# Kernel optimization log

Measured on AMD Instinct MI355X. Metric: run time of the kernel, lower is better.

Reference implementation:

```python
import jax, jax.numpy as jnp
import numpy as np

N_NODES = 50000
N_EDGES = 500000
D = 128  # in_size == out_size


def setup_inputs() -> dict:
    key = jax.random.key(0)
    ks = jax.random.split(key, 12)
    s = 1.0 / np.sqrt(D)
    feats = jax.random.normal(ks[0], (N_NODES, D), dtype=jnp.float32)
    # per-etype Linear params (torch Linear: y = x @ W.T + b)
    W_chem = jax.random.uniform(ks[1], (D, D), jnp.float32, -s, s)
    b_chem = jax.random.uniform(ks[2], (D,), jnp.float32, -s, s)
    W_elec = jax.random.uniform(ks[3], (D, D), jnp.float32, -s, s)
    b_elec = jax.random.uniform(ks[4], (D,), jnp.float32, -s, s)
    W_out = jax.random.uniform(ks[5], (D, D), jnp.float32, -s, s)
    b_out = jax.random.uniform(ks[6], (D,), jnp.float32, -s, s)
    src_chem = jax.random.randint(ks[7], (N_EDGES,), 0, N_NODES, dtype=jnp.int32)
    dst_chem = jax.random.randint(ks[8], (N_EDGES,), 0, N_NODES, dtype=jnp.int32)
    src_elec = jax.random.randint(ks[9], (N_EDGES,), 0, N_NODES, dtype=jnp.int32)
    dst_elec = jax.random.randint(ks[10], (N_EDGES,), 0, N_NODES, dtype=jnp.int32)
    return {
        "feats": feats,
        "W_chem": W_chem, "b_chem": b_chem,
        "W_elec": W_elec, "b_elec": b_elec,
        "W_out": W_out, "b_out": b_out,
        "src_chem": src_chem, "dst_chem": dst_chem,
        "src_elec": src_elec, "dst_elec": dst_elec,
    }


def reference(feats, W_chem, b_chem, W_elec, b_elec, W_out, b_out,
              src_chem, dst_chem, src_elec, dst_elec):
    n = feats.shape[0]
    # Per-etype linear projection of all node features
    Wh_chem = feats @ W_chem.T + b_chem  # [N, D]
    Wh_elec = feats @ W_elec.T + b_elec  # [N, D]
    # copy_src + sum scatter-aggregation per etype, merged with 'sum'
    h = jax.ops.segment_sum(Wh_chem[src_chem], dst_chem, num_segments=n)
    h = h + jax.ops.segment_sum(Wh_elec[src_elec], dst_elec, num_segments=n)
    # output Linear plus the last-iterated etype's Wh (quirk of original code:
    # 'electrical' is last in etypes order)
    return h @ W_out.T + b_out + Wh_elec
```

## Files before the change

### kernel.cpp

```cpp
#include <hip/hip_runtime.h>

#define D 128
#define PAD 48

typedef __attribute__((ext_vector_type(8))) short bf16x8;
typedef __attribute__((ext_vector_type(4))) float f32x4;

__device__ __forceinline__ unsigned short f2bf(float x) {
    unsigned int u = __float_as_uint(x);
    u += 0x7fffu + ((u >> 16) & 1u);
    return (unsigned short)(u >> 16);
}
__device__ __forceinline__ unsigned int pk2(float lo, float hi) {
    return ((unsigned int)f2bf(hi) << 16) | (unsigned int)f2bf(lo);
}
__device__ __forceinline__ float bf_lo(unsigned int u) { return __uint_as_float(u << 16); }
__device__ __forceinline__ float bf_hi(unsigned int u) { return __uint_as_float(u & 0xffff0000u); }

#define ACC8(U, P, Q)                                   \
        P.x += bf_lo(U.x); P.y += bf_hi(U.x);           \
        P.z += bf_lo(U.y); P.w += bf_hi(U.y);           \
        Q.x += bf_lo(U.z); Q.y += bf_hi(U.z);           \
        Q.z += bf_lo(U.w); Q.w += bf_hi(U.w);

__device__ __forceinline__ void agg_row(const unsigned short* __restrict__ fbf,
                                        const unsigned short* __restrict__ csr,
                                        const int* __restrict__ cnt,
                                        unsigned short* __restrict__ S,
                                        int v, int off) {
    const int deg = min(cnt[v], PAD);
    const unsigned short* row = csr + (size_t)v * PAD;
    float4 a0 = make_float4(0.f,0.f,0.f,0.f), b0 = make_float4(0.f,0.f,0.f,0.f);
    float4 a1 = make_float4(0.f,0.f,0.f,0.f), b1 = make_float4(0.f,0.f,0.f,0.f);
    float4 a2 = make_float4(0.f,0.f,0.f,0.f), b2 = make_float4(0.f,0.f,0.f,0.f);
    float4 a3 = make_float4(0.f,0.f,0.f,0.f), b3 = make_float4(0.f,0.f,0.f,0.f);
    int e = 0;
    for (; e + 4 <= deg; e += 4) {
        int i0 = row[e + 0];
        int i1 = row[e + 1];
        int i2 = row[e + 2];
        int i3 = row[e + 3];
        uint4 u0 = *(const uint4*)(fbf + (size_t)i0 * D + off);
        uint4 u1 = *(const uint4*)(fbf + (size_t)i1 * D + off);
        uint4 u2 = *(const uint4*)(fbf + (size_t)i2 * D + off);
        uint4 u3 = *(const uint4*)(fbf + (size_t)i3 * D + off);
        ACC8(u0, a0, b0) ACC8(u1, a1, b1) ACC8(u2, a2, b2) ACC8(u3, a3, b3)
    }
    for (; e < deg; ++e) {
        int sv = row[e];
        uint4 u = *(const uint4*)(fbf + (size_t)sv * D + off);
        ACC8(u, a0, b0)
    }
    a0.x += a1.x + a2.x + a3.x;  a0.y += a1.y + a2.y + a3.y;
    a0.z += a1.z + a2.z + a3.z;  a0.w += a1.w + a2.w + a3.w;
    b0.x += b1.x + b2.x + b3.x;  b0.y += b1.y + b2.y + b3.y;
    b0.z += b1.z + b2.z + b3.z;  b0.w += b1.w + b2.w + b3.w;
    uint4 o;
    o.x = pk2(a0.x, a0.y); o.y = pk2(a0.z, a0.w);
    o.z = pk2(b0.x, b0.y); o.w = pk2(b0.z, b0.w);
    *(uint4*)(S + (size_t)v * D + off) = o;
}

__global__ __launch_bounds__(256) void wzero(
    const float* __restrict__ Wc, const float* __restrict__ We,
    const float* __restrict__ Wo, const float* __restrict__ b_c,
    const float* __restrict__ b_e, const float* __restrict__ b_o,
    unsigned short* __restrict__ wall, float* __restrict__ bco,
    float* __restrict__ beo, float* __restrict__ bsum,
    int* __restrict__ cnt, int nzero) {
    const int id = blockIdx.x * 256 + threadIdx.x;
    for (int i = id; i < nzero; i += gridDim.x * 256) cnt[i] = 0;
    if (id < 16384) {
        const int j = id >> 7, k = id & 127;
        float s1 = 0.f, s2 = 0.f;
        for (int m = 0; m < 128; ++m) {
            float wo = Wo[j * 128 + m];
            s1 = fmaf(wo, Wc[m * 128 + k], s1);
            s2 = fmaf(wo, We[m * 128 + k], s2);
        }
        wall[j * 128 + k]         = f2bf(s1);
        wall[16384 + j * 128 + k] = f2bf(s2);
        wall[32768 + j * 128 + k] = f2bf(We[j * 128 + k]);
        if (k == 0) {
            float t1 = 0.f, t2 = 0.f;
            for (int m = 0; m < 128; ++m) {
                float wo = Wo[j * 128 + m];
                t1 = fmaf(wo, b_c[m], t1);
                t2 = fmaf(wo, b_e[m], t2);
            }
            bco[j] = t1; beo[j] = t2; bsum[j] = b_o[j] + b_e[j];
        }
    }
}

__global__ __launch_bounds__(256) void fillcv(
    const float4* __restrict__ f, uint4* __restrict__ o, int n8,
    const int* __restrict__ sc, const int* __restrict__ dc,
    int* __restrict__ cnt, unsigned short* __restrict__ csr, int E) {
    int i = blockIdx.x * 256 + threadIdx.x;
    if (i < n8) {
        float4 a = f[2 * i];
        float4 b = f[2 * i + 1];
        o[i] = make_uint4(pk2(a.x, a.y), pk2(a.z, a.w), pk2(b.x, b.y), pk2(b.z, b.w));
    }
    if (i < E) {
        int d = dc[i], s = sc[i];
        int pos = atomicAdd(&cnt[d], 1);
        if (pos < PAD) csr[(size_t)d * PAD + pos] = (unsigned short)s;
    }
}

__global__ __launch_bounds__(256) void fe_ac(
    const unsigned short* __restrict__ fbf,
    const int* __restrict__ se, const int* __restrict__ de,
    int* __restrict__ cnt, unsigned short* __restrict__ csr,
    unsigned short* __restrict__ S,
    int E, int N, int nf, int total) {
    const int bid = blockIdx.x;
    const int f0 = (int)(((long long)bid * nf) / total);
    const int f1 = (int)(((long long)(bid + 1) * nf) / total);
    if (f1 > f0) {
        const int i = f0 * 256 + threadIdx.x;
        if (i < E) {
            int d = de[i] + N, s = se[i];
            int pos = atomicAdd(&cnt[d], 1);
            if (pos < PAD) csr[(size_t)d * PAD + pos] = (unsigned short)s;
        }
    } else {
        const int aidx = bid - f0;
        const int wv  = threadIdx.x >> 6;
        const int ln  = threadIdx.x & 63;
        const int sub = ln >> 4;
        const int l16 = ln & 15;
        const int v = aidx * 16 + wv * 4 + sub;
        if (v < N) agg_row(fbf, csr, cnt, S, v, l16 * 8);
    }
}

__global__ __launch_bounds__(1024) void aggregate_bf(const unsigned short* __restrict__ fbf,
                                                     const unsigned short* __restrict__ csr,
                                                     const int* __restrict__ cnt,
                                                     unsigned short* __restrict__ S,
                                                     int base, int nend) {
    const int wv  = threadIdx.x >> 6;
    const int ln  = threadIdx.x & 63;
    const int sub = ln >> 4;
    const int l16 = ln & 15;
    const int v   = base + blockIdx.x * 64 + wv * 4 + sub;
    if (v < nend) agg_row(fbf, csr, cnt, S, v, l16 * 8);
}

__global__ __launch_bounds__(1024, 4) void gemm_w(
    const unsigned short* __restrict__ S,
    const unsigned short* __restrict__ fbf,
    const unsigned short* __restrict__ wall,
    const float* __restrict__ bco, const float* __restrict__ beo,
    const float* __restrict__ bsum,
    const int* __restrict__ degc, const int* __restrict__ dege,
    float* __restrict__ out, int M) {
    __shared__ unsigned int Wt[128 * 64];

    const int t    = threadIdx.x;
    const int r0   = blockIdx.x * 256;
    const int w    = t >> 6;
    const int lane = t & 63;
    const int ln   = lane & 15;
    const int quad = lane >> 4;
    const int lnx  = ln & 7;

    const int r      = r0 + w * 16 + ln;
    const bool valid = (r < M);

    f32x4 acc[8];
#pragma unroll
    for (int g = 0; g < 8; ++g) acc[g] = (f32x4){0.f, 0.f, 0.f, 0.f};

    const bf16x8 azero = {0, 0, 0, 0, 0, 0, 0, 0};

    const unsigned short* ap0 = S + (size_t)r * 128 + quad * 8;
    const unsigned short* ap1 = S + (size_t)(M + r) * 128 + quad * 8;
    const unsigned short* ap2 = fbf + (size_t)r * 128 + quad * 8;

#define STAGEB(P)                                                               \
    {                                                                           \
        const unsigned short* wp = wall + (size_t)(P) * 16384;                  \
        _Pragma("unroll") for (int i2 = 0; i2 < 2; ++i2) {                      \
            int g2 = i2 * 1024 + t;                                             \
            int j  = g2 >> 4;                                                   \
            int cc = g2 & 15;                                                   \
            uint4 v = *(const uint4*)(wp + (size_t)j * 128 + cc * 8);           \
            *(uint4*)(Wt + j * 64 + ((cc ^ (j & 7)) << 2)) = v;                 \
        }                                                                       \
    }

#define PHASE(AP)                                                                    \
    {                                                                                \
        bf16x8 a[4];                                                                 \
        _Pragma("unroll") for (int ks = 0; ks < 4; ++ks)                             \
            a[ks] = valid ? *(const bf16x8*)((AP) + ks * 32) : azero;                \
        _Pragma("unroll") for (int ks = 0; ks < 4; ++ks) {                           \
            const int cx = (((ks * 4 + quad) ^ lnx) << 2);                           \
            _Pragma("unroll") for (int g = 0; g < 8; ++g) {                          \
                bf16x8 b = *(const bf16x8*)(Wt + (g * 16 + ln) * 64 + cx);           \
                acc[g] = __builtin_amdgcn_mfma_f32_16x16x32_bf16(a[ks], b, acc[g],   \
                                                                 0, 0, 0);           \
            }                                                                        \
        }                                                                            \
    }

    STAGEB(0)
    __syncthreads();
    PHASE(ap0)
    __syncthreads();
    STAGEB(1)
    __syncthreads();
    PHASE(ap1)
    __syncthreads();
    STAGEB(2)
    __syncthreads();
    PHASE(ap2)
#undef PHASE
#undef STAGEB

    float dcv[4], dev[4];
    int   rrv[4];
#pragma unroll
    for (int rg = 0; rg < 4; ++rg) {
        const int rr = r0 + w * 16 + quad * 4 + rg;
        rrv[rg] = rr;
        dcv[rg] = (rr < M) ? (float)degc[rr] : 0.f;
        dev[rg] = (rr < M) ? (float)dege[rr] : 0.f;
    }
#pragma unroll
    for (int g = 0; g < 8; ++g) {
        const int col = g * 16 + ln;
        const float bc = bco[col], be = beo[col], bs = bsum[col];
#pragma unroll
        for (int rg = 0; rg < 4; ++rg) {
            if (rrv[rg] < M) {
                out[(size_t)rrv[rg] * 128 + col] =
                    acc[g][rg] + bs + dcv[rg] * bc + dev[rg] * be;
            }
        }
    }
}


extern "C" void kernel_launch(void* const* d_in, const int* in_sizes, int n_in,
                              void* d_out, int out_size, void* d_ws, size_t ws_size,
                              hipStream_t stream) {
    const float* feats  = (const float*)d_in[0];
    const float* W_chem = (const float*)d_in[1];
    const float* b_chem = (const float*)d_in[2];
    const float* W_elec = (const float*)d_in[3];
    const float* b_elec = (const float*)d_in[4];
    const float* W_out  = (const float*)d_in[5];
    const float* b_out  = (const float*)d_in[6];
    const int* src_chem = (const int*)d_in[7];
    const int* dst_chem = (const int*)d_in[8];
    const int* src_elec = (const int*)d_in[9];
    const int* dst_elec = (const int*)d_in[10];
    float* out = (float*)d_out;

    const int N = in_sizes[0] / D;
    const int E = in_sizes[7];
    const int N2 = 2 * N;

    unsigned short* fbf  = (unsigned short*)d_ws;
    unsigned short* S    = fbf + (size_t)N * D;
    unsigned short* wall = S + (size_t)N2 * D;
    float* bco  = (float*)(wall + 3 * 16384);
    float* beo  = bco + 128;
    float* bsum = beo + 128;
    int* cnt    = (int*)(bsum + 128);
    unsigned short* csr = (unsigned short*)(cnt + N2);

    const int n8 = N * D / 8;
    const int nf = (E + 255) / 256;
    const int na = (N + 15) / 16;
    const int total = nf + na;

    wzero<<<512, 256, 0, stream>>>(W_chem, W_elec, W_out, b_chem, b_elec, b_out,
                                   wall, bco, beo, bsum, cnt, N2);
    fillcv<<<(n8 + 255) / 256, 256, 0, stream>>>(
        (const float4*)feats, (uint4*)fbf, n8, src_chem, dst_chem, cnt, csr, E);
    fe_ac<<<total, 256, 0, stream>>>(fbf, src_elec, dst_elec, cnt, csr, S,
                                     E, N, nf, total);
    aggregate_bf<<<(N + 63) / 64, 1024, 0, stream>>>(fbf, csr, cnt, S, N, N2);
    gemm_w<<<(N + 255) / 256, 1024, 0, stream>>>(S, fbf, wall, bco, beo, bsum,
                                                 cnt, cnt + N, out, N);
}
```

Measured before the change: 221.2 us.

## Overlap elec aggregation with partial chem/self GEMM in one fused launch

Splits the final GEMM into two parts. The chem-aggregate and self-feature terms now run in the same launch as the elec-edge aggregation, with blocks interleaved, so the matmul work overlaps the gather-bound aggregation. A separate small GEMM then adds the elec-aggregate term into the output with a read-modify-write. This trades one extra pass over the output (read plus write of fp32) for the overlap, and block size drops from 1024 to 512 threads.

```diff
diff --git a/kernel.cpp b/kernel.cpp
--- a/kernel.cpp
+++ b/kernel.cpp
@@ -61,6 +61,33 @@
     *(uint4*)(S + (size_t)v * D + off) = o;
 }
 
+#define STAGEB(P, NT)                                                           \
+    {                                                                           \
+        const unsigned short* wp = wall + (size_t)(P) * 16384;                  \
+        _Pragma("unroll") for (int i2 = 0; i2 < 2048 / (NT); ++i2) {            \
+            int g2 = i2 * (NT) + t;                                             \
+            int j  = g2 >> 4;                                                   \
+            int cc = g2 & 15;                                                   \
+            uint4 v = *(const uint4*)(wp + (size_t)j * 128 + cc * 8);           \
+            *(uint4*)(Wt + j * 64 + ((cc ^ (j & 7)) << 2)) = v;                 \
+        }                                                                       \
+    }
+
+#define PHASE(AP)                                                                    \
+    {                                                                                \
+        bf16x8 a[4];                                                                 \
+        _Pragma("unroll") for (int ks = 0; ks < 4; ++ks)                             \
+            a[ks] = valid ? *(const bf16x8*)((AP) + ks * 32) : azero;                \
+        _Pragma("unroll") for (int ks = 0; ks < 4; ++ks) {                           \
+            const int cx = (((ks * 4 + quad) ^ lnx) << 2);                           \
+            _Pragma("unroll") for (int g = 0; g < 8; ++g) {                          \
+                bf16x8 b = *(const bf16x8*)(Wt + (g * 16 + ln) * 64 + cx);           \
+                acc[g] = __builtin_amdgcn_mfma_f32_16x16x32_bf16(a[ks], b, acc[g],   \
+                                                                 0, 0, 0);           \
+            }                                                                        \
+        }                                                                            \
+    }
+
 __global__ __launch_bounds__(256) void wzero(
     const float* __restrict__ Wc, const float* __restrict__ We,
     const float* __restrict__ Wo, const float* __restrict__ b_c,
@@ -137,109 +164,111 @@
     }
 }
 
-__global__ __launch_bounds__(1024) void aggregate_bf(const unsigned short* __restrict__ fbf,
-                                                     const unsigned short* __restrict__ csr,
-                                                     const int* __restrict__ cnt,
-                                                     unsigned short* __restrict__ S,
-                                                     int base, int nend) {
-    const int wv  = threadIdx.x >> 6;
-    const int ln  = threadIdx.x & 63;
-    const int sub = ln >> 4;
-    const int l16 = ln & 15;
-    const int v   = base + blockIdx.x * 64 + wv * 4 + sub;
-    if (v < nend) agg_row(fbf, csr, cnt, S, v, l16 * 8);
-}
-
-__global__ __launch_bounds__(1024, 4) void gemm_w(
-    const unsigned short* __restrict__ S,
+__global__ __launch_bounds__(512, 4) void ae_g02(
     const unsigned short* __restrict__ fbf,
+    const unsigned short* __restrict__ csr,
+    const int* __restrict__ cnt,
+    unsigned short* __restrict__ S,
     const unsigned short* __restrict__ wall,
     const float* __restrict__ bco, const float* __restrict__ beo,
     const float* __restrict__ bsum,
-    const int* __restrict__ degc, const int* __restrict__ dege,
+    float* __restrict__ out, int M, int ng, int total) {
+    __shared__ unsigned int Wt[128 * 64];
+    const int bid = blockIdx.x;
+    const int t   = threadIdx.x;
+    const int f0  = (int)(((long long)bid * ng) / total);
+    const int f1  = (int)(((long long)(bid + 1) * ng) / total);
+    if (f1 > f0) {
+        const int r0   = f0 * 128;
+        const int w    = t >> 6;
+        const int lane = t & 63;
+        const int ln   = lane & 15;
+        const int quad = lane >> 4;
+        const int lnx  = ln & 7;
+        const int r      = r0 + w * 16 + ln;
+        const bool valid = (r < M);
+        const bf16x8 azero = {0, 0, 0, 0, 0, 0, 0, 0};
+        const unsigned short* ap0 = S + (size_t)r * 128 + quad * 8;
+        const unsigned short* ap2 = fbf + (size_t)r * 128 + quad * 8;
+
+        f32x4 acc[8];
+#pragma unroll
+        for (int g = 0; g < 8; ++g) acc[g] = (f32x4){0.f, 0.f, 0.f, 0.f};
+
+        STAGEB(0, 512)
+        __syncthreads();
+        PHASE(ap0)
+        __syncthreads();
+        STAGEB(2, 512)
+        __syncthreads();
+        PHASE(ap2)
+
+        float dcv[4], dev[4];
+        int   rrv[4];
+#pragma unroll
+        for (int rg = 0; rg < 4; ++rg) {
+            const int rr = r0 + w * 16 + quad * 4 + rg;
+            rrv[rg] = rr;
+            dcv[rg] = (rr < M) ? (float)cnt[rr] : 0.f;
+            dev[rg] = (rr < M) ? (float)cnt[M + rr] : 0.f;
+        }
+#pragma unroll
+        for (int g = 0; g < 8; ++g) {
+            const int col = g * 16 + ln;
+            const float bc = bco[col], be = beo[col], bs = bsum[col];
+#pragma unroll
+            for (int rg = 0; rg < 4; ++rg) {
+                if (rrv[rg] < M) {
+                    out[(size_t)rrv[rg] * 128 + col] =
+                        acc[g][rg] + bs + dcv[rg] * bc + dev[rg] * be;
+                }
+            }
+        }
+    } else {
+        const int aidx = bid - f0;
+        const int wv  = t >> 6;
+        const int ln  = t & 63;
+        const int sub = ln >> 4;
+        const int l16 = ln & 15;
+        const int v = M + aidx * 32 + wv * 4 + sub;
+        if (v < 2 * M) agg_row(fbf, csr, cnt, S, v, l16 * 8);
+    }
+}
+
+__global__ __launch_bounds__(512, 4) void gemm_se(
+    const unsigned short* __restrict__ S,
+    const unsigned short* __restrict__ wall,
     float* __restrict__ out, int M) {
     __shared__ unsigned int Wt[128 * 64];
-
     const int t    = threadIdx.x;
-    const int r0   = blockIdx.x * 256;
+    const int r0   = blockIdx.x * 128;
     const int w    = t >> 6;
     const int lane = t & 63;
     const int ln   = lane & 15;
     const int quad = lane >> 4;
     const int lnx  = ln & 7;
-
     const int r      = r0 + w * 16 + ln;
     const bool valid = (r < M);
+    const bf16x8 azero = {0, 0, 0, 0, 0, 0, 0, 0};
+    const unsigned short* ap1 = S + (size_t)(M + r) * 128 + quad * 8;
 
     f32x4 acc[8];
 #pragma unroll
     for (int g = 0; g < 8; ++g) acc[g] = (f32x4){0.f, 0.f, 0.f, 0.f};
 
-    const bf16x8 azero = {0, 0, 0, 0, 0, 0, 0, 0};
-
-    const unsigned short* ap0 = S + (size_t)r * 128 + quad * 8;
-    const unsigned short* ap1 = S + (size_t)(M + r) * 128 + quad * 8;
-    const unsigned short* ap2 = fbf + (size_t)r * 128 + quad * 8;
-
-#define STAGEB(P)                                                               \
-    {                                                                           \
-        const unsigned short* wp = wall + (size_t)(P) * 16384;                  \
-        _Pragma("unroll") for (int i2 = 0; i2 < 2; ++i2) {                      \
-            int g2 = i2 * 1024 + t;                                             \
-            int j  = g2 >> 4;                                                   \
-            int cc = g2 & 15;                                                   \
-            uint4 v = *(const uint4*)(wp + (size_t)j * 128 + cc * 8);           \
-            *(uint4*)(Wt + j * 64 + ((cc ^ (j & 7)) << 2)) = v;                 \
-        }                                                                       \
-    }
-
-#define PHASE(AP)                                                                    \
-    {                                                                                \
-        bf16x8 a[4];                                                                 \
-        _Pragma("unroll") for (int ks = 0; ks < 4; ++ks)                             \
-            a[ks] = valid ? *(const bf16x8*)((AP) + ks * 32) : azero;                \
-        _Pragma("unroll") for (int ks = 0; ks < 4; ++ks) {                           \
-            const int cx = (((ks * 4 + quad) ^ lnx) << 2);                           \
-            _Pragma("unroll") for (int g = 0; g < 8; ++g) {                          \
-                bf16x8 b = *(const bf16x8*)(Wt + (g * 16 + ln) * 64 + cx);           \
-                acc[g] = __builtin_amdgcn_mfma_f32_16x16x32_bf16(a[ks], b, acc[g],   \
-                                                                 0, 0, 0);           \
-            }                                                                        \
-        }                                                                            \
-    }
-
-    STAGEB(0)
-    __syncthreads();
-    PHASE(ap0)
-    __syncthreads();
-    STAGEB(1)
+    STAGEB(1, 512)
     __syncthreads();
     PHASE(ap1)
-    __syncthreads();
-    STAGEB(2)
-    __syncthreads();
-    PHASE(ap2)
-#undef PHASE
-#undef STAGEB
-
-    float dcv[4], dev[4];
-    int   rrv[4];
-#pragma unroll
-    for (int rg = 0; rg < 4; ++rg) {
-        const int rr = r0 + w * 16 + quad * 4 + rg;
-        rrv[rg] = rr;
-        dcv[rg] = (rr < M) ? (float)degc[rr] : 0.f;
-        dev[rg] = (rr < M) ? (float)dege[rr] : 0.f;
-    }
+
 #pragma unroll
     for (int g = 0; g < 8; ++g) {
         const int col = g * 16 + ln;
-        const float bc = bco[col], be = beo[col], bs = bsum[col];
 #pragma unroll
         for (int rg = 0; rg < 4; ++rg) {
-            if (rrv[rg] < M) {
-                out[(size_t)rrv[rg] * 128 + col] =
-                    acc[g][rg] + bs + dcv[rg] * bc + dev[rg] * be;
+            const int rr = r0 + w * 16 + quad * 4 + rg;
+            if (rr < M) {
+                float* p = out + (size_t)rr * 128 + col;
+                *p = *p + acc[g][rg];
             }
         }
     }
@@ -278,15 +307,19 @@
     const int n8 = N * D / 8;
     const int nf = (E + 255) / 256;
     const int na = (N + 15) / 16;
-    const int total = nf + na;
+    const int total1 = nf + na;
+
+    const int ng = (N + 127) / 128;
+    const int na2 = (N + 31) / 32;
+    const int total2 = ng + na2;
 
     wzero<<<512, 256, 0, stream>>>(W_chem, W_elec, W_out, b_chem, b_elec, b_out,
                                    wall, bco, beo, bsum, cnt, N2);
     fillcv<<<(n8 + 255) / 256, 256, 0, stream>>>(
         (const float4*)feats, (uint4*)fbf, n8, src_chem, dst_chem, cnt, csr, E);
-    fe_ac<<<total, 256, 0, stream>>>(fbf, src_elec, dst_elec, cnt, csr, S,
-                                     E, N, nf, total);
-    aggregate_bf<<<(N + 63) / 64, 1024, 0, stream>>>(fbf, csr, cnt, S, N, N2);
-    gemm_w<<<(N + 255) / 256, 1024, 0, stream>>>(S, fbf, wall, bco, beo, bsum,
-                                                 cnt, cnt + N, out, N);
-}
+    fe_ac<<<total1, 256, 0, stream>>>(fbf, src_elec, dst_elec, cnt, csr, S,
+                                      E, N, nf, total1);
+    ae_g02<<<total2, 512, 0, stream>>>(fbf, csr, cnt, S, wall, bco, beo, bsum,
+                                       out, N, ng, total2);
+    gemm_se<<<ng, 512, 0, stream>>>(S, wall, out, N);
+}
```

Result: slower. 228.1 us (+3.1%).
